# Kernel tuning notes

Hardware: AMD Instinct MI355X
Metric: run time of the kernel (lower is better)

## Reference

```python
import jax, jax.numpy as jnp
import numpy as np
import math
from jax import lax

B, C, L = 16, 512, 1024
NCONV, K, H = 4, 7, 8
DH = C // H


def setup_inputs() -> dict:
    key = jax.random.key(0)
    ks = jax.random.split(key, 8)
    s = 0.02
    return {
        "inputx": jax.random.normal(ks[0], (B, C, L), jnp.float32),
        "mask": jnp.ones((B, L), jnp.int32),
        "number_of_layers": 1,
        "blocks": 1,
        "norm_c_scale": jnp.ones((NCONV, C), jnp.float32),
        "norm_c_bias": jnp.zeros((NCONV, C), jnp.float32),
        "dw_w": jax.random.normal(ks[1], (NCONV, C, K), jnp.float32) * s,
        "pw_w": jax.random.normal(ks[2], (NCONV, C, C), jnp.float32) * s,
        "pw_b": jnp.zeros((NCONV, C), jnp.float32),
        "ln1_s": jnp.ones((C,), jnp.float32),
        "ln1_b": jnp.zeros((C,), jnp.float32),
        "ln2_s": jnp.ones((C,), jnp.float32),
        "ln2_b": jnp.zeros((C,), jnp.float32),
        "w_kv": jax.random.normal(ks[3], (2 * C, C), jnp.float32) * s,
        "w_q": jax.random.normal(ks[4], (C, C), jnp.float32) * s,
        "ffn1_w": jax.random.normal(ks[5], (C, C), jnp.float32) * s,
        "ffn1_b": jnp.zeros((C,), jnp.float32),
        "ffn2_w": jax.random.normal(ks[6], (C, C), jnp.float32) * s,
        "ffn2_b": jnp.zeros((C,), jnp.float32),
    }


def _ln(x, s, b, eps=1e-5):  # x: [B, L, C], normalize over C
    mu = jnp.mean(x, axis=-1, keepdims=True)
    var = jnp.mean((x - mu) ** 2, axis=-1, keepdims=True)
    return (x - mu) * lax.rsqrt(var + eps) * s + b


def _ln_ch(x, s, b):  # x: [B, C, L] -> LayerNorm over channel dim
    return _ln(x.transpose(0, 2, 1), s, b).transpose(0, 2, 1)


def _pos_enc(x, minimum=1.0, maximum=10000.0):  # x: [B, C, L]
    xt = x.transpose(0, 2, 1)  # [B, L, C]
    ns = C // 2
    log_inc = math.log(maximum / minimum) / (ns - 1)
    inv = minimum * jnp.exp(jnp.arange(ns, dtype=jnp.float32) * -log_inc)
    pos = jnp.arange(L, dtype=jnp.float32)
    scaled = pos[:, None] * inv[None, :]  # [L, ns]
    sig = jnp.concatenate([jnp.sin(scaled), jnp.cos(scaled)], axis=1)  # [L, 2*ns]
    if C % 2 == 1:
        sig = jnp.pad(sig, ((0, 0), (0, 1)))
    return (xt + sig[None]).transpose(0, 2, 1)


def _conv1x1(w, x, b=None):  # w: [O, I], x: [B, I, L]
    y = jnp.einsum('oi,bil->bol', w, x)
    if b is not None:
        y = y + b[:, None]
    return y


def _dwconv(x, w):  # x: [B, C, L], w: [C, K], groups=C, same padding
    return lax.conv_general_dilated(
        x, w[:, None, :], window_strides=(1,), padding=[(K // 2, K // 2)],
        feature_group_count=C, dimension_numbers=('NCH', 'OIH', 'NCH'))


def _attention(x, mask, w_kv, w_q):  # x: [B, C, L]
    kv = _conv1x1(w_kv, x).transpose(0, 2, 1)  # [B, L, 2C]
    q = _conv1x1(w_q, x).transpose(0, 2, 1)    # [B, L, C]
    k, v = kv[..., :C], kv[..., C:]

    def split(t):  # [B, L, C] -> [B, H, L, DH]
        return t.reshape(B, L, H, DH).transpose(0, 2, 1, 3)

    q, k, v = split(q) * (DH ** -0.5), split(k), split(v)
    logits = jnp.einsum('bhqd,bhkd->bhqk', q, k)
    maskf = mask[:, None, None, :].astype(jnp.float32)
    logits = logits + (-1e30) * (1.0 - maskf)
    w = jax.nn.softmax(logits, axis=-1)
    o = jnp.einsum('bhqk,bhkd->bhqd', w, v)
    return o.transpose(0, 2, 1, 3).reshape(B, L, C).transpose(0, 2, 1)


def reference(inputx, mask, number_of_layers, blocks, norm_c_scale, norm_c_bias,
              dw_w, pw_w, pw_b, ln1_s, ln1_b, ln2_s, ln2_b, w_kv, w_q,
              ffn1_w, ffn1_b, ffn2_w, ffn2_b):
    # Eval-mode forward: dropout and stochastic depth are identity.
    result = _pos_enc(inputx)
    for i in range(NCONV):
        res = result
        h = _ln_ch(result, norm_c_scale[i], norm_c_bias[i])
        h = _dwconv(h, dw_w[i])
        h = jax.nn.relu(_conv1x1(pw_w[i], h, pw_b[i]))
        result = h + res
    res = result
    h = _ln_ch(result, ln1_s, ln1_b)
    result = _attention(h, mask, w_kv, w_q) + res
    res = result
    h = _ln_ch(result, ln2_s, ln2_b)
    h = jax.nn.relu(_conv1x1(ffn1_w, h, ffn1_b))
    h = _conv1x1(ffn2_w, h, ffn2_b)
    return h + res
```

## Files before the change

### kernel.cpp

```cpp
#include <hip/hip_runtime.h>
#include <math.h>

#define BB 16
#define CC 512
#define LL 1024
#define NCONV 4
#define KW 7
#define NH 8
#define DH 64

typedef short short8 __attribute__((ext_vector_type(8)));
typedef float f32x4  __attribute__((ext_vector_type(4)));

union bfpack2 { __bf16 h[2]; unsigned u; };
union bfpack4 { __bf16 h[4]; uint2 v; };
union bfpack8 { __bf16 h[8]; uint4 v; };

__device__ __forceinline__ void gload_lds16(const void* g, void* l) {
    __builtin_amdgcn_global_load_lds(
        (const __attribute__((address_space(1))) void*)g,
        (__attribute__((address_space(3))) void*)l, 16, 0, 0);
}

__global__ __launch_bounds__(256) void wprep_kernel(
    const float* __restrict__ pw, const float* __restrict__ wkv,
    const float* __restrict__ wq, const float* __restrict__ f1,
    const float* __restrict__ f2, __bf16* __restrict__ out)
{
    const int S = CC * CC;
    int i = (blockIdx.x * 256 + threadIdx.x) * 4;
    const float* src; int base;
    if (i < 4 * S)      { src = pw;  base = 0; }
    else if (i < 6 * S) { src = wkv; base = 4 * S; }
    else if (i < 7 * S) { src = wq;  base = 6 * S; }
    else if (i < 8 * S) { src = f1;  base = 7 * S; }
    else                { src = f2;  base = 8 * S; }
    float4 f = *(const float4*)(src + (i - base));
    bfpack4 p;
    p.h[0] = (__bf16)f.x; p.h[1] = (__bf16)f.y;
    p.h[2] = (__bf16)f.z; p.h[3] = (__bf16)f.w;
    *(uint2*)(out + i) = p.v;
}

__global__ __launch_bounds__(256) void dw_transpose_kernel(
    const float* __restrict__ w, __bf16* __restrict__ wt)
{
    int t = blockIdx.x * 256 + threadIdx.x;
    if (t < NCONV * KW * CC) {
        int c = t & (CC - 1);
        int k = (t >> 9) % KW;
        int i = t / (KW * CC);
        wt[t] = (__bf16)w[(i * CC + c) * KW + k];
    }
}

__global__ __launch_bounds__(256) void pos_enc_t_kernel(
    const float* __restrict__ x, float* __restrict__ out)
{
    __shared__ float T[64 * 65];
    const int b = blockIdx.z, c0 = blockIdx.y * 64, l0 = blockIdx.x * 64;
    const int t = threadIdx.x;
    {
        int lt = t & 63, cr0 = t >> 6;
        #pragma unroll
        for (int j = 0; j < 16; ++j) {
            int cr = cr0 + 4 * j;
            T[cr * 65 + lt] = x[((size_t)b * CC + c0 + cr) * LL + l0 + lt];
        }
    }
    __syncthreads();
    {
        int ct = t & 63, lr0 = t >> 6;
        const float log_inc = 0.03611898185f;
        int c = c0 + ct;
        int half = (c < CC / 2) ? c : c - CC / 2;
        float inv = __expf(-log_inc * (float)half);
        #pragma unroll
        for (int j = 0; j < 16; ++j) {
            int lr = lr0 + 4 * j;
            int l = l0 + lr;
            float ph = (float)l * inv;
            float sig = (c < CC / 2) ? __sinf(ph) : __cosf(ph);
            out[((size_t)b * LL + l) * CC + c] = T[ct * 65 + lr] + sig;
        }
    }
}

__global__ __launch_bounds__(256) void ln_last_kernel(
    const float* __restrict__ x, const float* __restrict__ gam,
    const float* __restrict__ bet, __bf16* __restrict__ out)
{
    int row = blockIdx.x * 4 + (threadIdx.x >> 6);
    int ln = threadIdx.x & 63;
    const float* xr = x + (size_t)row * CC + ln * 8;
    float4 a = *(const float4*)xr;
    float4 c = *(const float4*)(xr + 4);
    float sum = a.x + a.y + a.z + a.w + c.x + c.y + c.z + c.w;
    float sq  = a.x*a.x + a.y*a.y + a.z*a.z + a.w*a.w
              + c.x*c.x + c.y*c.y + c.z*c.z + c.w*c.w;
    #pragma unroll
    for (int off = 1; off < 64; off <<= 1) {
        sum += __shfl_xor(sum, off);
        sq  += __shfl_xor(sq, off);
    }
    float mean = sum * (1.0f / CC);
    float rstd = rsqrtf(sq * (1.0f / CC) - mean * mean + 1e-5f);
    float4 g0 = *(const float4*)(gam + ln * 8);
    float4 g1 = *(const float4*)(gam + ln * 8 + 4);
    float4 b0 = *(const float4*)(bet + ln * 8);
    float4 b1 = *(const float4*)(bet + ln * 8 + 4);
    bfpack8 p;
    p.h[0] = (__bf16)((a.x - mean) * rstd * g0.x + b0.x);
    p.h[1] = (__bf16)((a.y - mean) * rstd * g0.y + b0.y);
    p.h[2] = (__bf16)((a.z - mean) * rstd * g0.z + b0.z);
    p.h[3] = (__bf16)((a.w - mean) * rstd * g0.w + b0.w);
    p.h[4] = (__bf16)((c.x - mean) * rstd * g1.x + b1.x);
    p.h[5] = (__bf16)((c.y - mean) * rstd * g1.y + b1.y);
    p.h[6] = (__bf16)((c.z - mean) * rstd * g1.z + b1.z);
    p.h[7] = (__bf16)((c.w - mean) * rstd * g1.w + b1.w);
    *(uint4*)(out + (size_t)row * CC + ln * 8) = p.v;
}

__global__ __launch_bounds__(256) void ln_dw_kernel(
    const float* __restrict__ x, const float* __restrict__ gam,
    const float* __restrict__ bet, const __bf16* __restrict__ wt,
    __bf16* __restrict__ out)
{
    __shared__ __attribute__((aligned(16))) __bf16 Hs[40][CC];
    const int b = blockIdx.y;
    const int l0 = blockIdx.x * 32;
    const int t = threadIdx.x;
    const int w = t >> 6, ln = t & 63;

    float4 g0 = *(const float4*)(gam + ln * 8);
    float4 g1 = *(const float4*)(gam + ln * 8 + 4);
    float4 bb0 = *(const float4*)(bet + ln * 8);
    float4 bb1 = *(const float4*)(bet + ln * 8 + 4);

    #pragma unroll
    for (int p = 0; p < 10; ++p) {
        int ri = p * 4 + w;
        int l = l0 - 4 + ri;
        if (l < 0 || l >= LL) {
            uint4 z = {0u, 0u, 0u, 0u};
            *(uint4*)(&Hs[ri][ln * 8]) = z;
        } else {
            const float* xr = x + ((size_t)b * LL + l) * CC + ln * 8;
            float4 a = *(const float4*)xr;
            float4 c = *(const float4*)(xr + 4);
            float sum = a.x + a.y + a.z + a.w + c.x + c.y + c.z + c.w;
            float sq  = a.x*a.x + a.y*a.y + a.z*a.z + a.w*a.w
                      + c.x*c.x + c.y*c.y + c.z*c.z + c.w*c.w;
            #pragma unroll
            for (int off = 1; off < 64; off <<= 1) {
                sum += __shfl_xor(sum, off);
                sq  += __shfl_xor(sq, off);
            }
            float mean = sum * (1.0f / CC);
            float rstd = rsqrtf(sq * (1.0f / CC) - mean * mean + 1e-5f);
            bfpack8 pp;
            pp.h[0] = (__bf16)((a.x - mean) * rstd * g0.x + bb0.x);
            pp.h[1] = (__bf16)((a.y - mean) * rstd * g0.y + bb0.y);
            pp.h[2] = (__bf16)((a.z - mean) * rstd * g0.z + bb0.z);
            pp.h[3] = (__bf16)((a.w - mean) * rstd * g0.w + bb0.w);
            pp.h[4] = (__bf16)((c.x - mean) * rstd * g1.x + bb1.x);
            pp.h[5] = (__bf16)((c.y - mean) * rstd * g1.y + bb1.y);
            pp.h[6] = (__bf16)((c.z - mean) * rstd * g1.z + bb1.z);
            pp.h[7] = (__bf16)((c.w - mean) * rstd * g1.w + bb1.w);
            *(uint4*)(&Hs[ri][ln * 8]) = pp.v;
        }
    }
    __syncthreads();

    const int cc0 = (t & 63) * 8;
    bfpack8 wv[KW];
    #pragma unroll
    for (int k = 0; k < KW; ++k) wv[k].v = *(const uint4*)(wt + k * CC + cc0);
    #pragma unroll
    for (int j = 0; j < 8; ++j) {
        int r = (t >> 6) + 4 * j;
        float acc[8] = {};
        #pragma unroll
        for (int k = 0; k < KW; ++k) {
            bfpack8 xv;
            xv.v = *(const uint4*)(&Hs[r + 1 + k][cc0]);
            #pragma unroll
            for (int i2 = 0; i2 < 8; ++i2)
                acc[i2] += (float)xv.h[i2] * (float)wv[k].h[i2];
        }
        bfpack8 o;
        #pragma unroll
        for (int i2 = 0; i2 < 8; ++i2) o.h[i2] = (__bf16)acc[i2];
        *(uint4*)(out + ((size_t)b * LL + l0 + r) * CC + cc0) = o.v;
    }
}

__global__ __launch_bounds__(256) void gemm_bf_kernel(
    const __bf16* __restrict__ Wm, const __bf16* __restrict__ X,
    void* __restrict__ Yv, const float* __restrict__ bias,
    const float* __restrict__ res, const int mode, const int relu,
    const float scale)
{
    const int b  = blockIdx.z;
    const int l0 = blockIdx.x * 128;
    const int o0 = blockIdx.y * 128;
    const __bf16* Xb = X + (size_t)b * LL * CC;

    __shared__ __attribute__((aligned(16))) __bf16 Al0[128 * 64];
    __shared__ __attribute__((aligned(16))) __bf16 Al1[128 * 64];
    __shared__ __attribute__((aligned(16))) __bf16 Bl0[128 * 64];
    __shared__ __attribute__((aligned(16))) __bf16 Bl1[128 * 64];

    const int tid = threadIdx.x;
    const int wave = tid >> 6, lane = tid & 63;
    const int wm = wave >> 1, wn = wave & 1;
    const int ln = lane & 15, kq = lane >> 4;

    const int swapped = (mode >= 2);
    const __bf16* Aptr = swapped ? (Xb + (size_t)l0 * CC) : (Wm + (size_t)o0 * CC);
    const __bf16* Bptr = swapped ? (Wm + (size_t)o0 * CC) : (Xb + (size_t)l0 * CC);

    f32x4 acc[4][4] = {};

    const int srow  = tid >> 3;
    const int sc    = ((tid & 7) ^ (srow & 7)) * 8;
    const int lbase = wave * 8 * 64;

    auto STAGE = [&](__bf16* Ad, __bf16* Bd, int k0) {
        #pragma unroll
        for (int j = 0; j < 4; ++j) {
            gload_lds16(Aptr + (size_t)(j * 32 + srow) * CC + k0 + sc,
                        Ad + j * 32 * 64 + lbase);
            gload_lds16(Bptr + (size_t)(j * 32 + srow) * CC + k0 + sc,
                        Bd + j * 32 * 64 + lbase);
        }
    };
    auto COMPUTE = [&](const __bf16* As, const __bf16* Bs) {
        #pragma unroll
        for (int kk = 0; kk < 2; ++kk) {
            const int so = ((kk * 4 + kq) ^ (ln & 7)) * 8;
            short8 af[4], bfr[4];
            #pragma unroll
            for (int mi = 0; mi < 4; ++mi)
                af[mi] = *(const short8*)(As + (wm * 64 + mi * 16 + ln) * 64 + so);
            #pragma unroll
            for (int ni = 0; ni < 4; ++ni)
                bfr[ni] = *(const short8*)(Bs + (wn * 64 + ni * 16 + ln) * 64 + so);
            #pragma unroll
            for (int mi = 0; mi < 4; ++mi)
                #pragma unroll
                for (int ni = 0; ni < 4; ++ni)
                    acc[mi][ni] = __builtin_amdgcn_mfma_f32_16x16x32_bf16(
                        af[mi], bfr[ni], acc[mi][ni], 0, 0, 0);
        }
    };

    STAGE(Al0, Bl0, 0);
    __syncthreads();
    #pragma unroll
    for (int k0 = 0; k0 < CC; k0 += 128) {
        STAGE(Al1, Bl1, k0 + 64);
        COMPUTE(Al0, Bl0);
        __syncthreads();
        if (k0 + 128 < CC) {
            STAGE(Al0, Bl0, k0 + 128);
            COMPUTE(Al1, Bl1);
            __syncthreads();
        } else {
            COMPUTE(Al1, Bl1);
        }
    }

    if (mode == 0) {
        float* Y = (float*)Yv;
        #pragma unroll
        for (int mi = 0; mi < 4; ++mi) {
            int cb = o0 + wm * 64 + mi * 16 + kq * 4;
            #pragma unroll
            for (int ni = 0; ni < 4; ++ni) {
                int l = l0 + wn * 64 + ni * 16 + ln;
                size_t idx = ((size_t)b * LL + l) * CC + cb;
                float4 r4 = *(const float4*)(Y + idx);
                float4 v;
                v.x = fmaxf(acc[mi][ni][0] + bias[cb + 0], 0.f) + r4.x;
                v.y = fmaxf(acc[mi][ni][1] + bias[cb + 1], 0.f) + r4.y;
                v.z = fmaxf(acc[mi][ni][2] + bias[cb + 2], 0.f) + r4.z;
                v.w = fmaxf(acc[mi][ni][3] + bias[cb + 3], 0.f) + r4.w;
                *(float4*)(Y + idx) = v;
            }
        }
    } else if (mode == 1) {
        __bf16* Y = (__bf16*)Yv;
        #pragma unroll
        for (int mi = 0; mi < 4; ++mi) {
            int cb = o0 + wm * 64 + mi * 16 + kq * 4;
            #pragma unroll
            for (int ni = 0; ni < 4; ++ni) {
                int l = l0 + wn * 64 + ni * 16 + ln;
                bfpack4 p;
                #pragma unroll
                for (int i = 0; i < 4; ++i) {
                    float v = acc[mi][ni][i] * scale;
                    if (bias) v += bias[cb + i];
                    if (relu) v = fmaxf(v, 0.f);
                    p.h[i] = (__bf16)v;
                }
                *(uint2*)(Y + ((size_t)b * LL + l) * CC + cb) = p.v;
            }
        }
    } else {
        float* Y = (float*)Yv;
        #pragma unroll
        for (int mi = 0; mi < 4; ++mi) {
            int lb = l0 + wm * 64 + mi * 16 + kq * 4;
            #pragma unroll
            for (int ni = 0; ni < 4; ++ni) {
                int c = o0 + wn * 64 + ni * 16 + ln;
                float bv = bias[c];
                const float* rp = res + ((size_t)b * LL + lb) * CC + c;
                float4 v;
                v.x = acc[mi][ni][0] + bv + rp[0 * CC];
                v.y = acc[mi][ni][1] + bv + rp[1 * CC];
                v.z = acc[mi][ni][2] + bv + rp[2 * CC];
                v.w = acc[mi][ni][3] + bv + rp[3 * CC];
                *(float4*)(Y + ((size_t)b * CC + c) * LL + lb) = v;
            }
        }
    }
}

__global__ __launch_bounds__(256) void qkv_gemm_kernel(
    const __bf16* __restrict__ wkv, const __bf16* __restrict__ wq,
    const __bf16* __restrict__ X, __bf16* __restrict__ kout,
    __bf16* __restrict__ vout, __bf16* __restrict__ qout)
{
    const int b  = blockIdx.z;
    const int l0 = blockIdx.x * 128;
    const int sel = blockIdx.y >> 2;
    const int o0 = (blockIdx.y & 3) * 128;
    const __bf16* Xb = X + (size_t)b * LL * CC;
    const __bf16* Wsel = (sel == 0) ? wkv : (sel == 1 ? wkv + CC * CC : wq);

    __shared__ __attribute__((aligned(16))) __bf16 Al0[128 * 64];
    __shared__ __attribute__((aligned(16))) __bf16 Al1[128 * 64];
    __shared__ __attribute__((aligned(16))) __bf16 Bl0[128 * 64];
    __shared__ __attribute__((aligned(16))) __bf16 Bl1[128 * 64];

    const int tid = threadIdx.x;
    const int wave = tid >> 6, lane = tid & 63;
    const int wm = wave >> 1, wn = wave & 1;
    const int ln = lane & 15, kq = lane >> 4;

    const int swapped = (sel == 1);
    const __bf16* Aptr = swapped ? (Xb + (size_t)l0 * CC) : (Wsel + (size_t)o0 * CC);
    const __bf16* Bptr = swapped ? (Wsel + (size_t)o0 * CC) : (Xb + (size_t)l0 * CC);

    f32x4 acc[4][4] = {};

    const int srow  = tid >> 3;
    const int sc    = ((tid & 7) ^ (srow & 7)) * 8;
    const int lbase = wave * 8 * 64;

    auto STAGE = [&](__bf16* Ad, __bf16* Bd, int k0) {
        #pragma unroll
        for (int j = 0; j < 4; ++j) {
            gload_lds16(Aptr + (size_t)(j * 32 + srow) * CC + k0 + sc,
                        Ad + j * 32 * 64 + lbase);
            gload_lds16(Bptr + (size_t)(j * 32 + srow) * CC + k0 + sc,
                        Bd + j * 32 * 64 + lbase);
        }
    };
    auto COMPUTE = [&](const __bf16* As, const __bf16* Bs) {
        #pragma unroll
        for (int kk = 0; kk < 2; ++kk) {
            const int so = ((kk * 4 + kq) ^ (ln & 7)) * 8;
            short8 af[4], bfr[4];
            #pragma unroll
            for (int mi = 0; mi < 4; ++mi)
                af[mi] = *(const short8*)(As + (wm * 64 + mi * 16 + ln) * 64 + so);
            #pragma unroll
            for (int ni = 0; ni < 4; ++ni)
                bfr[ni] = *(const short8*)(Bs + (wn * 64 + ni * 16 + ln) * 64 + so);
            #pragma unroll
            for (int mi = 0; mi < 4; ++mi)
                #pragma unroll
                for (int ni = 0; ni < 4; ++ni)
                    acc[mi][ni] = __builtin_amdgcn_mfma_f32_16x16x32_bf16(
                        af[mi], bfr[ni], acc[mi][ni], 0, 0, 0);
        }
    };

    STAGE(Al0, Bl0, 0);
    __syncthreads();
    #pragma unroll
    for (int k0 = 0; k0 < CC; k0 += 128) {
        STAGE(Al1, Bl1, k0 + 64);
        COMPUTE(Al0, Bl0);
        __syncthreads();
        if (k0 + 128 < CC) {
            STAGE(Al0, Bl0, k0 + 128);
            COMPUTE(Al1, Bl1);
            __syncthreads();
        } else {
            COMPUTE(Al1, Bl1);
        }
    }

    if (sel == 1) {
        #pragma unroll
        for (int mi = 0; mi < 4; ++mi) {
            int lb = l0 + wm * 64 + mi * 16 + kq * 4;
            #pragma unroll
            for (int ni = 0; ni < 4; ++ni) {
                int c = o0 + wn * 64 + ni * 16 + ln;
                bfpack4 p;
                #pragma unroll
                for (int i = 0; i < 4; ++i) p.h[i] = (__bf16)acc[mi][ni][i];
                *(uint2*)(vout + ((size_t)b * CC + c) * LL + lb) = p.v;
            }
        }
    } else {
        __bf16* Y = (sel == 0) ? kout : qout;
        const float scale = (sel == 0) ? 1.0f : 0.18033688011f;
        #pragma unroll
        for (int mi = 0; mi < 4; ++mi) {
            int cb = o0 + wm * 64 + mi * 16 + kq * 4;
            #pragma unroll
            for (int ni = 0; ni < 4; ++ni) {
                int l = l0 + wn * 64 + ni * 16 + ln;
                bfpack4 p;
                #pragma unroll
                for (int i = 0; i < 4; ++i)
                    p.h[i] = (__bf16)(acc[mi][ni][i] * scale);
                *(uint2*)(Y + ((size_t)b * LL + l) * CC + cb) = p.v;
            }
        }
    }
}

__global__ __launch_bounds__(256) void attn_mfma_kernel(
    const __bf16* __restrict__ qb, const __bf16* __restrict__ kb,
    const __bf16* __restrict__ vb, const int* __restrict__ maskp,
    float* __restrict__ outp)
{
    const int b = blockIdx.z, hh = blockIdx.y, ql0 = blockIdx.x * 64;
    const int tid = threadIdx.x, w = tid >> 6, lane = tid & 63;
    const int ln = lane & 15, kq = lane >> 4;

    __shared__ __attribute__((aligned(16))) __bf16 K0l[64 * 64];
    __shared__ __attribute__((aligned(16))) __bf16 K1l[64 * 64];
    __shared__ __attribute__((aligned(16))) __bf16 V0l[64 * 64];
    __shared__ __attribute__((aligned(16))) __bf16 V1l[64 * 64];
    __shared__ __attribute__((aligned(16))) __bf16 Pl [64 * 64];

    const int co = hh * 64;
    const int srow = tid >> 3, slot = tid & 7;

    short8 qf[2];
    #pragma unroll
    for (int c = 0; c < 2; ++c)
        qf[c] = *(const short8*)(qb + ((size_t)b * LL + ql0 + w * 16 + ln) * CC
                                 + co + c * 32 + kq * 8);

    float l_run = 0.f;
    f32x4 oacc[4] = {};

    auto STAGE = [&](__bf16* Kd, __bf16* Vd, int m0) {
        #pragma unroll
        for (int j = 0; j < 2; ++j) {
            int row = srow + 32 * j;
            int gs = (slot ^ (row & 7)) * 8;
            gload_lds16(kb + ((size_t)b * LL + m0 + row) * CC + co + gs,
                        Kd + j * 2048 + w * 512);
            gload_lds16(vb + ((size_t)(b * CC + co + row)) * LL + m0 + gs,
                        Vd + j * 2048 + w * 512);
        }
    };

    auto TILE = [&](const __bf16* Kc, const __bf16* Vc, int m0) {
        f32x4 s[4] = {};
        __builtin_amdgcn_s_setprio(1);
        #pragma unroll
        for (int ni = 0; ni < 4; ++ni)
            #pragma unroll
            for (int c = 0; c < 2; ++c) {
                short8 bk = *(const short8*)(Kc + (ni * 16 + ln) * 64
                                             + (((c * 4 + kq) ^ (ln & 7)) * 8));
                s[ni] = __builtin_amdgcn_mfma_f32_16x16x32_bf16(bk, qf[c], s[ni], 0, 0, 0);
            }
        __builtin_amdgcn_s_setprio(0);

        #pragma unroll
        for (int ni = 0; ni < 4; ++ni) {
            int4 mv = *(const int4*)(maskp + b * LL + m0 + ni * 16 + kq * 4);
            float p0 = exp2f(mv.x ? s[ni][0] : -1e30f);
            float p1 = exp2f(mv.y ? s[ni][1] : -1e30f);
            float p2 = exp2f(mv.z ? s[ni][2] : -1e30f);
            float p3 = exp2f(mv.w ? s[ni][3] : -1e30f);
            l_run += (p0 + p1) + (p2 + p3);
            bfpack4 p4;
            p4.h[0] = (__bf16)p0; p4.h[1] = (__bf16)p1;
            p4.h[2] = (__bf16)p2; p4.h[3] = (__bf16)p3;
            int s16 = (2 * ni + (kq >> 1)) ^ (ln & 7);
            *(uint2*)(Pl + (w * 16 + ln) * 64 + s16 * 8 + (kq & 1) * 4) = p4.v;
        }
        asm volatile("s_waitcnt lgkmcnt(0)" ::: "memory");

        short8 bp[2];
        #pragma unroll
        for (int c = 0; c < 2; ++c)
            bp[c] = *(const short8*)(Pl + (w * 16 + ln) * 64
                                     + (((c * 4 + kq) ^ (ln & 7)) * 8));
        __builtin_amdgcn_s_setprio(1);
        #pragma unroll
        for (int ni = 0; ni < 4; ++ni)
            #pragma unroll
            for (int c = 0; c < 2; ++c) {
                short8 av = *(const short8*)(Vc + (ni * 16 + ln) * 64
                                             + (((c * 4 + kq) ^ (ln & 7)) * 8));
                oacc[ni] = __builtin_amdgcn_mfma_f32_16x16x32_bf16(av, bp[c], oacc[ni], 0, 0, 0);
            }
        __builtin_amdgcn_s_setprio(0);
    };

    STAGE(K0l, V0l, 0);
    for (int m0 = 0; m0 < LL; m0 += 128) {
        __syncthreads();
        if (m0 + 64 < LL) STAGE(K1l, V1l, m0 + 64);
        TILE(K0l, V0l, m0);
        __syncthreads();
        if (m0 + 128 < LL) STAGE(K0l, V0l, m0 + 128);
        TILE(K1l, V1l, m0 + 64);
    }

    l_run += __shfl_xor(l_run, 16);
    l_run += __shfl_xor(l_run, 32);
    float inv = 1.0f / l_run;

    int l = ql0 + w * 16 + ln;
    #pragma unroll
    for (int ni = 0; ni < 4; ++ni) {
        int c = co + ni * 16 + kq * 4;
        size_t idx = ((size_t)b * LL + l) * CC + c;
        float4 r4 = *(const float4*)(outp + idx);
        r4.x += oacc[ni][0] * inv;
        r4.y += oacc[ni][1] * inv;
        r4.z += oacc[ni][2] * inv;
        r4.w += oacc[ni][3] * inv;
        *(float4*)(outp + idx) = r4;
    }
}

extern "C" void kernel_launch(void* const* d_in, const int* in_sizes, int n_in,
                              void* d_out, int out_size, void* d_ws, size_t ws_size,
                              hipStream_t stream)
{
    const float* inputx  = (const float*)d_in[0];
    const int*   mask    = (const int*)  d_in[1];
    const float* ncs     = (const float*)d_in[4];
    const float* ncb     = (const float*)d_in[5];
    const float* dw_w    = (const float*)d_in[6];
    const float* pw_w    = (const float*)d_in[7];
    const float* pw_b    = (const float*)d_in[8];
    const float* ln1_s   = (const float*)d_in[9];
    const float* ln1_b   = (const float*)d_in[10];
    const float* ln2_s   = (const float*)d_in[11];
    const float* ln2_b   = (const float*)d_in[12];
    const float* w_kv    = (const float*)d_in[13];
    const float* w_q     = (const float*)d_in[14];
    const float* ffn1_w  = (const float*)d_in[15];
    const float* ffn1_b  = (const float*)d_in[16];
    const float* ffn2_w  = (const float*)d_in[17];
    const float* ffn2_b  = (const float*)d_in[18];

    const size_t NT = (size_t)BB * CC * LL;
    float*  result = (float*)d_ws;
    __bf16* wsb  = (__bf16*)(result + NT);
    __bf16* hb   = wsb;
    __bf16* xb   = wsb + NT;
    __bf16* qbuf = wsb + 2 * NT;
    __bf16* kbuf = wsb + 3 * NT;
    __bf16* vbuf = wsb + 4 * NT;
    __bf16* wpw  = wsb + 5 * NT;
    __bf16* wkv  = wpw + 4 * CC * CC;
    __bf16* wq   = wkv + 2 * CC * CC;
    __bf16* wf1  = wq + CC * CC;
    __bf16* wf2  = wf1 + CC * CC;
    __bf16* dwt  = wf2 + CC * CC;

    dim3 blk(256);
    dim3 ggrid(LL / 128, CC / 128, BB);

    wprep_kernel<<<9 * CC * CC / 1024, blk, 0, stream>>>(pw_w, w_kv, w_q, ffn1_w, ffn2_w, wpw);
    dw_transpose_kernel<<<(NCONV * KW * CC + 255) / 256, blk, 0, stream>>>(dw_w, dwt);

    pos_enc_t_kernel<<<dim3(LL / 64, CC / 64, BB), blk, 0, stream>>>(inputx, result);

    for (int i = 0; i < NCONV; ++i) {
        ln_dw_kernel<<<dim3(LL / 32, BB), blk, 0, stream>>>(
            result, ncs + i * CC, ncb + i * CC, dwt + i * KW * CC, xb);
        gemm_bf_kernel<<<ggrid, blk, 0, stream>>>(wpw + (size_t)i * CC * CC, xb, result,
                                                  pw_b + i * CC, nullptr, 0, 1, 1.0f);
    }

    ln_last_kernel<<<BB * LL / 4, blk, 0, stream>>>(result, ln1_s, ln1_b, hb);
    qkv_gemm_kernel<<<dim3(LL / 128, 12, BB), blk, 0, stream>>>(wkv, wq, hb, kbuf, vbuf, qbuf);
    attn_mfma_kernel<<<dim3(LL / 64, NH, BB), blk, 0, stream>>>(qbuf, kbuf, vbuf, mask, result);

    ln_last_kernel<<<BB * LL / 4, blk, 0, stream>>>(result, ln2_s, ln2_b, hb);
    gemm_bf_kernel<<<ggrid, blk, 0, stream>>>(wf1, hb, xb, ffn1_b, nullptr, 1, 1, 1.0f);
    gemm_bf_kernel<<<ggrid, blk, 0, stream>>>(wf2, xb, d_out, ffn2_b, result, 2, 0, 1.0f);
}
```

Before: 439.8 us.

## Replace LDS double-buffering with register-prefetched K/V tiles in attention

New measurement: 434.5 us. No clear change (-1.2%).

```diff
diff --git a/kernel.cpp b/kernel.cpp
--- a/kernel.cpp
+++ b/kernel.cpp
@@ -447,14 +447,13 @@
     const int tid = threadIdx.x, w = tid >> 6, lane = tid & 63;
     const int ln = lane & 15, kq = lane >> 4;
 
-    __shared__ __attribute__((aligned(16))) __bf16 K0l[64 * 64];
-    __shared__ __attribute__((aligned(16))) __bf16 K1l[64 * 64];
-    __shared__ __attribute__((aligned(16))) __bf16 V0l[64 * 64];
-    __shared__ __attribute__((aligned(16))) __bf16 V1l[64 * 64];
-    __shared__ __attribute__((aligned(16))) __bf16 Pl [64 * 64];
+    __shared__ __attribute__((aligned(16))) __bf16 Kl[64 * 64];
+    __shared__ __attribute__((aligned(16))) __bf16 Vl[64 * 64];
+    __shared__ __attribute__((aligned(16))) __bf16 Pl[64 * 64];
 
     const int co = hh * 64;
-    const int srow = tid >> 3, slot = tid & 7;
+    const int sr = tid >> 3, slot = tid & 7;
+    const int wslot = slot ^ (sr & 7);
 
     short8 qf[2];
     #pragma unroll
@@ -465,26 +464,34 @@
     float l_run = 0.f;
     f32x4 oacc[4] = {};
 
-    auto STAGE = [&](__bf16* Kd, __bf16* Vd, int m0) {
-        #pragma unroll
-        for (int j = 0; j < 2; ++j) {
-            int row = srow + 32 * j;
-            int gs = (slot ^ (row & 7)) * 8;
-            gload_lds16(kb + ((size_t)b * LL + m0 + row) * CC + co + gs,
-                        Kd + j * 2048 + w * 512);
-            gload_lds16(vb + ((size_t)(b * CC + co + row)) * LL + m0 + gs,
-                        Vd + j * 2048 + w * 512);
-        }
-    };
-
-    auto TILE = [&](const __bf16* Kc, const __bf16* Vc, int m0) {
+    uint4 kv0, kv1, vv0, vv1;
+    kv0 = *(const uint4*)(kb + ((size_t)b * LL + sr) * CC + co + slot * 8);
+    kv1 = *(const uint4*)(kb + ((size_t)b * LL + sr + 32) * CC + co + slot * 8);
+    vv0 = *(const uint4*)(vb + ((size_t)(b * CC + co + sr)) * LL + slot * 8);
+    vv1 = *(const uint4*)(vb + ((size_t)(b * CC + co + sr + 32)) * LL + slot * 8);
+
+    for (int m0 = 0; m0 < LL; m0 += 64) {
+        __syncthreads();
+        *(uint4*)(Kl + sr * 64 + wslot * 8)        = kv0;
+        *(uint4*)(Kl + (sr + 32) * 64 + wslot * 8) = kv1;
+        *(uint4*)(Vl + sr * 64 + wslot * 8)        = vv0;
+        *(uint4*)(Vl + (sr + 32) * 64 + wslot * 8) = vv1;
+        __syncthreads();
+        {
+            int mn = (m0 + 64 < LL) ? m0 + 64 : m0;
+            kv0 = *(const uint4*)(kb + ((size_t)b * LL + mn + sr) * CC + co + slot * 8);
+            kv1 = *(const uint4*)(kb + ((size_t)b * LL + mn + sr + 32) * CC + co + slot * 8);
+            vv0 = *(const uint4*)(vb + ((size_t)(b * CC + co + sr)) * LL + mn + slot * 8);
+            vv1 = *(const uint4*)(vb + ((size_t)(b * CC + co + sr + 32)) * LL + mn + slot * 8);
+        }
+
         f32x4 s[4] = {};
         __builtin_amdgcn_s_setprio(1);
         #pragma unroll
         for (int ni = 0; ni < 4; ++ni)
             #pragma unroll
             for (int c = 0; c < 2; ++c) {
-                short8 bk = *(const short8*)(Kc + (ni * 16 + ln) * 64
+                short8 bk = *(const short8*)(Kl + (ni * 16 + ln) * 64
                                              + (((c * 4 + kq) ^ (ln & 7)) * 8));
                 s[ni] = __builtin_amdgcn_mfma_f32_16x16x32_bf16(bk, qf[c], s[ni], 0, 0, 0);
             }
@@ -516,21 +523,11 @@
         for (int ni = 0; ni < 4; ++ni)
             #pragma unroll
             for (int c = 0; c < 2; ++c) {
-                short8 av = *(const short8*)(Vc + (ni * 16 + ln) * 64
+                short8 av = *(const short8*)(Vl + (ni * 16 + ln) * 64
                                              + (((c * 4 + kq) ^ (ln & 7)) * 8));
                 oacc[ni] = __builtin_amdgcn_mfma_f32_16x16x32_bf16(av, bp[c], oacc[ni], 0, 0, 0);
             }
         __builtin_amdgcn_s_setprio(0);
-    };
-
-    STAGE(K0l, V0l, 0);
-    for (int m0 = 0; m0 < LL; m0 += 128) {
-        __syncthreads();
-        if (m0 + 64 < LL) STAGE(K1l, V1l, m0 + 64);
-        TILE(K0l, V0l, m0);
-        __syncthreads();
-        if (m0 + 128 < LL) STAGE(K0l, V0l, m0 + 128);
-        TILE(K1l, V1l, m0 + 64);
     }
 
     l_run += __shfl_xor(l_run, 16);
```
